# Optimization experiments

Measured on AMD Instinct MI355X. Metric: run time of the kernel, lower is better.

Reference implementation:

```python
import jax, jax.numpy as jnp
import numpy as np
import math

NEG = -1e9


def maximum_path(neg_cent, text_len, spec_len):
    # neg_cent: [B, Ts, Tt]; monotonic alignment (Viterbi) DP as in VITS.
    B, Ts, Tt = neg_cent.shape
    jj = jnp.arange(Tt)
    tt = jnp.arange(Ts)
    node_mask = (jj[None, None, :] < text_len[:, None, None]) & (tt[None, :, None] < spec_len[:, None, None])
    nc = jnp.where(node_mask, neg_cent, NEG)

    def fstep(q, nc_t):
        # q: [B, Tt] best score ending at text index j at previous frame
        q_shift = jnp.concatenate([jnp.full((B, 1), NEG, q.dtype), q[:, :-1]], axis=1)
        d = q_shift >= q  # True -> came from j-1 (diagonal move)
        q_new = nc_t + jnp.maximum(q, q_shift)
        return q_new, d

    q0 = jnp.broadcast_to(jnp.where(jj == 0, 0.0, NEG), (B, Tt)).astype(neg_cent.dtype)
    _, dirs = jax.lax.scan(fstep, q0, jnp.swapaxes(nc, 0, 1))  # dirs: [Ts, B, Tt]

    def bstep(j, inp):
        t, d_t = inp
        start = (t == spec_len - 1)
        j_eff = jnp.where(start, text_len - 1, j)
        valid = t < spec_len
        emit = ((jj[None, :] == j_eff[:, None]) & valid[:, None]).astype(neg_cent.dtype)
        came_diag = jnp.take_along_axis(d_t, j_eff[:, None], axis=1)[:, 0]
        j_next = jnp.where(valid, jnp.maximum(j_eff - came_diag.astype(j_eff.dtype), 0), j_eff)
        return j_next, emit

    j_init = jnp.zeros((B,), text_len.dtype)
    _, path = jax.lax.scan(bstep, j_init, (jnp.arange(Ts), dirs), reverse=True)
    return jnp.swapaxes(path, 0, 1)  # [B, Ts, Tt]


def setup_inputs() -> dict:
    B, C, Ts, Tt = 16, 192, 2048, 512
    key = jax.random.key(0)
    k1, k2, k3, k4, k5 = jax.random.split(key, 5)
    z_p = jax.random.normal(k1, (B, C, Ts), dtype=jnp.float32)
    m_p = jax.random.normal(k2, (B, C, Tt), dtype=jnp.float32)
    logs_p = 0.1 * jax.random.normal(k3, (B, C, Tt), dtype=jnp.float32)
    text_len = jax.random.randint(k4, (B,), Tt // 2, Tt + 1, dtype=jnp.int32)
    extra = jax.random.randint(k5, (B,), 0, Ts - Tt + 1, dtype=jnp.int32)
    spec_len = jnp.minimum(text_len + extra, Ts)
    return {"z_p": z_p, "m_p": m_p, "logs_p": logs_p, "spec_len": spec_len, "text_len": text_len}


def reference(z_p, m_p, logs_p, spec_len, text_len):
    B, C, Ts = z_p.shape
    Tt = m_p.shape[2]
    text_mask = (jnp.arange(Tt)[None, :] < text_len[:, None]).astype(z_p.dtype)[:, None, :]  # [B,1,Tt]
    spec_mask = (jnp.arange(Ts)[None, :] < spec_len[:, None]).astype(z_p.dtype)[:, None, :]  # [B,1,Ts]

    # --- neg_cent (torch.no_grad block) ---
    s_p_sq_r = jnp.exp(-2.0 * logs_p)  # [B,C,Tt]
    neg_cent1 = jnp.sum(-0.5 * math.log(2.0 * math.pi) - logs_p, axis=1, keepdims=True)  # [B,1,Tt]
    neg_cent2 = jnp.einsum('bct,bcu->btu', -0.5 * z_p ** 2, s_p_sq_r)  # [B,Ts,Tt]
    neg_cent3 = jnp.einsum('bct,bcu->btu', z_p, m_p * s_p_sq_r)  # [B,Ts,Tt]
    neg_cent4 = jnp.sum(-0.5 * m_p ** 2 * s_p_sq_r, axis=1, keepdims=True)  # [B,1,Tt]
    neg_cent = neg_cent1 + neg_cent2 + neg_cent3 + neg_cent4

    path = jax.lax.stop_gradient(maximum_path(neg_cent, text_len, spec_len))  # [B,Ts,Tt]

    duration = jnp.sum(path, axis=1)[:, None, :]  # [B,1,Tt]
    logw_ = jnp.log(duration + 1e-6) * text_mask  # [B,1,Tt]

    # expand prior stats along the alignment path: [B,C,Ts]
    m_p_exp = jnp.einsum('btu,bcu->bct', path, m_p)
    logs_p_exp = jnp.einsum('btu,bcu->bct', path, logs_p)

    return (path, duration, logw_, m_p_exp, logs_p_exp, text_mask, spec_mask)
```

## Files before the change

### kernel.cpp

```cpp
#include <hip/hip_runtime.h>
#include <hip/hip_bf16.h>
#include <math.h>

#define BB 16
#define CC 192
#define TS 2048
#define TT 512
#define KK 384

#define OFF_PATH 0
#define OFF_DUR  (16777216)
#define OFF_LOGW (OFF_DUR + 8192)
#define OFF_MEXP (OFF_LOGW + 8192)
#define OFF_LEXP (OFF_MEXP + 6291456)
#define OFF_TMASK (OFF_LEXP + 6291456)
#define OFF_SMASK (OFF_TMASK + 8192)

#define NEGCF (-1e9f)

__global__ __launch_bounds__(512) void vits_prep(
    const float* __restrict__ m_p, const float* __restrict__ logs_p,
    const int* __restrict__ spec_len, const int* __restrict__ text_len,
    float* __restrict__ Bmat, float* __restrict__ avec,
    float* __restrict__ tmask, float* __restrict__ smask)
{
    const int uc = blockIdx.x;
    const int b  = blockIdx.y;
    const int tid = threadIdx.x;
    const int ul = tid & 31;
    const int cg = tid >> 5;
    const int u = uc*32 + ul;
    const float C0 = -0.91893853320467274178f;
    float a_acc = 0.f;
    for (int c = cg; c < CC; c += 16) {
        float lg = logs_p[((size_t)b*CC + c)*TT + u];
        float mm = m_p[((size_t)b*CC + c)*TT + u];
        float s  = expf(-2.f*lg);
        float ms = mm * s;
        Bmat[((size_t)b*KK + 2*c    )*TT + u] = ms;
        Bmat[((size_t)b*KK + 2*c + 1)*TT + u] = s;
        a_acc += C0 - lg - 0.5f*mm*ms;
    }
    __shared__ float red[16][33];
    red[cg][ul] = a_acc;
    __syncthreads();
    #pragma unroll
    for (int s = 8; s > 0; s >>= 1) {
        if (cg < s) red[cg][ul] += red[cg + s][ul];
        __syncthreads();
    }
    if (cg == 0) {
        avec[b*TT + u] = red[0][ul];
        tmask[b*TT + u] = (u < text_len[b]) ? 1.f : 0.f;
    }
    if (tid < 128) {
        int t = uc*128 + tid;
        smask[b*TS + t] = (t < spec_len[b]) ? 1.f : 0.f;
    }
}

__global__ __launch_bounds__(256) void vits_gemm(
    const float* __restrict__ z, const float* __restrict__ Bmat,
    const float* __restrict__ avec, float* __restrict__ out)
{
    const int b  = blockIdx.z;
    const int t0 = blockIdx.y * 128;
    const int u0 = blockIdx.x * 128;
    __shared__ float As[8][128];
    __shared__ float Bs[8][128];
    const int tid = threadIdx.x;
    const int tx = tid & 15, ty = tid >> 4;
    float acc[8][8] = {};
    const float* zb = z    + (size_t)b * CC * TS;
    const float* Bb = Bmat + (size_t)b * KK * TT;

    const int c_l = tid >> 6;
    const int t_l = (tid & 63) * 2;
    const int k_b = tid >> 5;
    const int u_l = (tid & 31) * 4;

    float2 zr = *(const float2*)(zb + (size_t)c_l*TS + t0 + t_l);
    float4 br = *(const float4*)(Bb + (size_t)k_b*TT + u0 + u_l);

    for (int kc = 0; kc < KK/8; ++kc) {
        *(float2*)&As[2*c_l  ][t_l] = make_float2(zr.x, zr.y);
        *(float2*)&As[2*c_l+1][t_l] = make_float2(-0.5f*zr.x*zr.x, -0.5f*zr.y*zr.y);
        *(float4*)&Bs[k_b][u_l] = br;
        __syncthreads();
        if (kc + 1 < KK/8) {
            zr = *(const float2*)(zb + (size_t)((kc+1)*4 + c_l)*TS + t0 + t_l);
            br = *(const float4*)(Bb + (size_t)((kc+1)*8 + k_b)*TT + u0 + u_l);
        }
        #pragma unroll
        for (int k = 0; k < 8; ++k) {
            float4 a0 = *(const float4*)&As[k][ty*4];
            float4 a1 = *(const float4*)&As[k][ty*4 + 64];
            float4 b0 = *(const float4*)&Bs[k][tx*4];
            float4 b1 = *(const float4*)&Bs[k][tx*4 + 64];
            float aa[8] = {a0.x,a0.y,a0.z,a0.w,a1.x,a1.y,a1.z,a1.w};
            float bb[8] = {b0.x,b0.y,b0.z,b0.w,b1.x,b1.y,b1.z,b1.w};
            #pragma unroll
            for (int i = 0; i < 8; ++i)
                #pragma unroll
                for (int j = 0; j < 8; ++j)
                    acc[i][j] += aa[i]*bb[j];
        }
        __syncthreads();
    }

    float4 ab0 = *(const float4*)(avec + b*TT + u0 + tx*4);
    float4 ab1 = *(const float4*)(avec + b*TT + u0 + tx*4 + 64);
    float ab[8] = {ab0.x,ab0.y,ab0.z,ab0.w,ab1.x,ab1.y,ab1.z,ab1.w};
    #pragma unroll
    for (int i = 0; i < 8; ++i) {
        int tt = t0 + ((i < 4) ? (ty*4 + i) : (64 + ty*4 + (i-4)));
        float* orow = out + (size_t)((size_t)b*TS + tt)*TT + u0;
        float4 o0, o1;
        o0.x = acc[i][0] + ab[0]; o0.y = acc[i][1] + ab[1];
        o0.z = acc[i][2] + ab[2]; o0.w = acc[i][3] + ab[3];
        o1.x = acc[i][4] + ab[4]; o1.y = acc[i][5] + ab[5];
        o1.z = acc[i][6] + ab[6]; o1.w = acc[i][7] + ab[7];
        *(float4*)(orow + tx*4)      = o0;
        *(float4*)(orow + tx*4 + 64) = o1;
    }
}

__device__ __forceinline__ float dpp_ror1_f32(float v) {
    union { float f; int i; } u, r;
    u.f = v;
    r.i = __builtin_amdgcn_update_dpp(0, u.i, 0x13C, 0xF, 0xF, false);
    return r.f;
}

#define DIRS(j,w) dirs[((j)<<6) | ((w) ^ ((j) & 31))]
#define RING 16

__global__ __launch_bounds__(1024, 1) void vits_dp(
    const float* __restrict__ nc,
    const int* __restrict__ spec_len, const int* __restrict__ text_len,
    float* __restrict__ dur, float* __restrict__ logw, int* __restrict__ jt)
{
    __shared__ unsigned int dirs[TT*(TS/32)];
    __shared__ float qrow[TT];
    __shared__ int Tr[TT + 1];

    const int tid  = threadIdx.x;
    const int lane = tid & 63;
    const int wid  = tid >> 6;
    const int b = blockIdx.x;
    const int SL = spec_len[b], TL = text_len[b];
    const int col = (wid << 5) + lane - 32;
    const bool auth = (lane >= 32);
    const bool w0g  = (wid == 0) && (lane < 32);
    const int colL = (col < 0) ? 0 : col;

    float q = (col == 0) ? 0.0f : NEGCF;
    unsigned int bits = 0;

    const float* ncb = nc + (size_t)b*TS*TT + colL;

    float pf[RING];
    #pragma unroll
    for (int i = 0; i < RING; ++i) pf[i] = ncb[(size_t)i*TT];
    const float* pcur = ncb + (size_t)RING*TT;

    int tb = 0;
    for (; tb + 32 <= SL; tb += 32) {
        #pragma unroll
        for (int s = 0; s < 32; ++s) {
            const int t = tb + s;
            float f = pf[s & (RING-1)];
            pf[s & (RING-1)] = *pcur;
            pcur += TT;

            float qp = dpp_ror1_f32(q);
            bool d = (qp >= q);
            bits = (bits << 1) | (unsigned)d;
            float qn = f + fmaxf(qp, q);
            q = w0g ? NEGCF : qn;

            if (s == 31) {
                if (auth) {
                    DIRS(col, t >> 5) = bits;
                    qrow[col] = q;
                }
                bits = 0;
                __syncthreads();
                if (!auth && wid != 0) q = qrow[col];
                __syncthreads();
            }
        }
    }
    for (int t = tb; t < SL; ++t) {
        float f = ncb[(size_t)t*TT];
        float qp = dpp_ror1_f32(q);
        bool d = (qp >= q);
        bits = (bits << 1) | (unsigned)d;
        float qn = f + fmaxf(qp, q);
        q = w0g ? NEGCF : qn;
    }
    if (SL & 31) {
        int w = SL >> 5, r = SL & 31;
        if (auth) DIRS(col, w) = bits << (32 - r);
    }
    __syncthreads();

    for (int i = tid; i <= TT; i += 1024) Tr[i] = 0;
    __syncthreads();

    if (tid == 0) {
        Tr[TL] = SL;
        int j = TL - 1, tc = SL - 1;
        while (j > 0 && tc >= 0) {
            int w = tc >> 5;
            int bcur = 31 - (tc & 31);
            unsigned int W = DIRS(j, w) & (0xFFFFFFFFu << bcur);
            if (W) {
                int bp = __ffs(W) - 1;
                int tp = (w << 5) + 31 - bp;
                Tr[j] = tp;
                --j;
                tc = tp - 1;
            } else {
                if (w == 0) break;
                tc = (w << 5) - 1;
            }
        }
    }
    __syncthreads();

    for (int u = tid; u < TT; u += 1024) {
        float dv = (u < TL) ? (float)(Tr[u+1] - Tr[u]) : 0.0f;
        dur[b*TT + u] = dv;
        logw[b*TT + u] = (u < TL) ? logf(dv + 1e-6f) : 0.0f;
    }
    for (int u = 0; u < TL; ++u) {
        int t1 = Tr[u+1];
        for (int t = Tr[u] + tid; t < t1; t += 1024) jt[b*TS + t] = u;
    }
    for (int t = SL + tid; t < TS; t += 1024) jt[b*TS + t] = -1;
}

__global__ void vits_path(const int* __restrict__ jt, float4* __restrict__ path)
{
    int idx = blockIdx.x*blockDim.x + threadIdx.x;
    const int total = BB*TS*(TT/4);
    for (; idx < total; idx += gridDim.x*blockDim.x) {
        int u4 = idx & (TT/4 - 1);
        int bt = idx >> 7;
        int j = jt[bt];
        float4 v = make_float4(0.f,0.f,0.f,0.f);
        int r = j - (u4 << 2);
        if (r >= 0 && r < 4) ((float*)&v)[r] = 1.f;
        path[idx] = v;
    }
}

__global__ void vits_mlexp(const int* __restrict__ jt,
    const float* __restrict__ m_p, const float* __restrict__ logs_p,
    float4* __restrict__ mexp, float4* __restrict__ lexp)
{
    int idx = blockIdx.x*blockDim.x + threadIdx.x;
    const int total = BB*CC*(TS/4);
    for (; idx < total; idx += gridDim.x*blockDim.x) {
        int t4 = idx & (TS/4 - 1);
        int bc = idx >> 9;
        int b = bc / CC;
        int4 jv = *(const int4*)(jt + b*TS + (t4 << 2));
        const float* mrow = m_p    + (size_t)bc*TT;
        const float* lrow = logs_p + (size_t)bc*TT;
        float4 mv, lv;
        mv.x = (jv.x >= 0) ? mrow[jv.x] : 0.f;  lv.x = (jv.x >= 0) ? lrow[jv.x] : 0.f;
        mv.y = (jv.y >= 0) ? mrow[jv.y] : 0.f;  lv.y = (jv.y >= 0) ? lrow[jv.y] : 0.f;
        mv.z = (jv.z >= 0) ? mrow[jv.z] : 0.f;  lv.z = (jv.z >= 0) ? lrow[jv.z] : 0.f;
        mv.w = (jv.w >= 0) ? mrow[jv.w] : 0.f;  lv.w = (jv.w >= 0) ? lrow[jv.w] : 0.f;
        mexp[idx] = mv;
        lexp[idx] = lv;
    }
}

extern "C" void kernel_launch(void* const* d_in, const int* in_sizes, int n_in,
                              void* d_out, int out_size, void* d_ws, size_t ws_size,
                              hipStream_t stream) {
    const float* z_p      = (const float*)d_in[0];
    const float* m_p      = (const float*)d_in[1];
    const float* logs_p   = (const float*)d_in[2];
    const int*   spec_len = (const int*)d_in[3];
    const int*   text_len = (const int*)d_in[4];
    float* out = (float*)d_out;

    float* Bmat = (float*)d_ws;
    float* avec = Bmat + (size_t)BB*KK*TT;
    int*   jt   = (int*)(avec + BB*TT);

    float* path  = out + OFF_PATH;
    float* dur   = out + OFF_DUR;
    float* logw  = out + OFF_LOGW;
    float* mexp  = out + OFF_MEXP;
    float* lexp  = out + OFF_LEXP;
    float* tmask = out + OFF_TMASK;
    float* smask = out + OFF_SMASK;

    vits_prep<<<dim3(16, BB), 512, 0, stream>>>(m_p, logs_p, spec_len, text_len,
                                                Bmat, avec, tmask, smask);
    vits_gemm<<<dim3(TT/128, TS/128, BB), 256, 0, stream>>>(z_p, Bmat, avec, path);
    vits_dp<<<BB, 1024, 0, stream>>>(path, spec_len, text_len, dur, logw, jt);
    vits_path<<<2048, 256, 0, stream>>>(jt, (float4*)path);
    vits_mlexp<<<2048, 256, 0, stream>>>(jt, m_p, logs_p, (float4*)mexp, (float4*)lexp);
}
```

Baseline: 440.8 us.

## Store cost matrix in time-grouped layout and stream DP rows through LDS ring

The GEMM epilogue now writes neg_cent in a transposed layout that groups four consecutive time steps per text column, as float4. The DP kernel streams these groups into a three-slot LDS ring using global_load_lds with explicit waitcnt and barrier control, replacing the per-thread register prefetch ring. This gives the serial scan one LDS float4 read per four steps and overlaps global loads with compute. The cost is more barriers per window, strided float4 stores in the GEMM epilogue, and Tr reusing ring memory.

```diff
diff --git a/kernel.cpp b/kernel.cpp
--- a/kernel.cpp
+++ b/kernel.cpp
@@ -17,6 +17,7 @@
 #define OFF_SMASK (OFF_TMASK + 8192)
 
 #define NEGCF (-1e9f)
+#define GSTR (TT*4)
 
 __global__ __launch_bounds__(512) void vits_prep(
     const float* __restrict__ m_p, const float* __restrict__ logs_p,
@@ -61,7 +62,7 @@
 
 __global__ __launch_bounds__(256) void vits_gemm(
     const float* __restrict__ z, const float* __restrict__ Bmat,
-    const float* __restrict__ avec, float* __restrict__ out)
+    const float* __restrict__ avec, float* __restrict__ ncT)
 {
     const int b  = blockIdx.z;
     const int t0 = blockIdx.y * 128;
@@ -111,17 +112,19 @@
     float4 ab0 = *(const float4*)(avec + b*TT + u0 + tx*4);
     float4 ab1 = *(const float4*)(avec + b*TT + u0 + tx*4 + 64);
     float ab[8] = {ab0.x,ab0.y,ab0.z,ab0.w,ab1.x,ab1.y,ab1.z,ab1.w};
+    float* ncTb = ncT + (size_t)b*(TS/4)*GSTR;
+    const int g1 = (t0 >> 2) + ty;
+    const int g2 = g1 + 16;
     #pragma unroll
-    for (int i = 0; i < 8; ++i) {
-        int tt = t0 + ((i < 4) ? (ty*4 + i) : (64 + ty*4 + (i-4)));
-        float* orow = out + (size_t)((size_t)b*TS + tt)*TT + u0;
-        float4 o0, o1;
-        o0.x = acc[i][0] + ab[0]; o0.y = acc[i][1] + ab[1];
-        o0.z = acc[i][2] + ab[2]; o0.w = acc[i][3] + ab[3];
-        o1.x = acc[i][4] + ab[4]; o1.y = acc[i][5] + ab[5];
-        o1.z = acc[i][6] + ab[6]; o1.w = acc[i][7] + ab[7];
-        *(float4*)(orow + tx*4)      = o0;
-        *(float4*)(orow + tx*4 + 64) = o1;
+    for (int jj = 0; jj < 8; ++jj) {
+        int u = u0 + ((jj < 4) ? (tx*4 + jj) : (64 + tx*4 + (jj-4)));
+        float4 lo, hi;
+        lo.x = acc[0][jj]+ab[jj]; lo.y = acc[1][jj]+ab[jj];
+        lo.z = acc[2][jj]+ab[jj]; lo.w = acc[3][jj]+ab[jj];
+        hi.x = acc[4][jj]+ab[jj]; hi.y = acc[5][jj]+ab[jj];
+        hi.z = acc[6][jj]+ab[jj]; hi.w = acc[7][jj]+ab[jj];
+        *(float4*)(ncTb + ((size_t)g1*TT + u)*4) = lo;
+        *(float4*)(ncTb + ((size_t)g2*TT + u)*4) = hi;
     }
 }
 
@@ -132,17 +135,20 @@
     return r.f;
 }
 
+#define GLDS(srcp, dstp) __builtin_amdgcn_global_load_lds( \
+    (const __attribute__((address_space(1))) unsigned int*)(srcp), \
+    (__attribute__((address_space(3))) unsigned int*)(dstp), 4, 0, 0)
+
 #define DIRS(j,w) dirs[((j)<<6) | ((w) ^ ((j) & 31))]
-#define RING 16
 
 __global__ __launch_bounds__(1024, 1) void vits_dp(
-    const float* __restrict__ nc,
+    const float* __restrict__ ncT,
     const int* __restrict__ spec_len, const int* __restrict__ text_len,
     float* __restrict__ dur, float* __restrict__ logw, int* __restrict__ jt)
 {
     __shared__ unsigned int dirs[TT*(TS/32)];
+    __shared__ float ring[3][2048];
     __shared__ float qrow[TT];
-    __shared__ int Tr[TT + 1];
 
     const int tid  = threadIdx.x;
     const int lane = tid & 63;
@@ -157,42 +163,58 @@
     float q = (col == 0) ? 0.0f : NEGCF;
     unsigned int bits = 0;
 
-    const float* ncb = nc + (size_t)b*TS*TT + colL;
-
-    float pf[RING];
-    #pragma unroll
-    for (int i = 0; i < RING; ++i) pf[i] = ncb[(size_t)i*TT];
-    const float* pcur = ncb + (size_t)RING*TT;
-
-    int tb = 0;
-    for (; tb + 32 <= SL; tb += 32) {
+    const char* ncB = (const char*)ncT + (size_t)b*(TS/4)*8192;
+    const int stoff = wid*512 + (lane << 2);
+
+    const int nwin = SL >> 2;
+
+    {
+        const char* s0 = ncB + stoff;
+        GLDS(s0,        (char*)&ring[0][0] + stoff);
+        GLDS(s0 + 256,  (char*)&ring[0][0] + stoff + 256);
+        const char* s1 = ncB + 8192 + stoff;
+        GLDS(s1,        (char*)&ring[1][0] + stoff);
+        GLDS(s1 + 256,  (char*)&ring[1][0] + stoff + 256);
+    }
+    asm volatile("s_waitcnt vmcnt(0)" ::: "memory");
+    __syncthreads();
+
+    int slot = 0;
+    for (int k = 0; k < nwin; ++k) {
+        asm volatile("s_barrier" ::: "memory");
+        {
+            int g = k + 2; if (g > TS/4 - 1) g = TS/4 - 1;
+            int s2 = slot + 2; if (s2 >= 3) s2 -= 3;
+            const char* sp = ncB + (size_t)g*8192 + stoff;
+            char* dp_ = (char*)&ring[0][0] + s2*8192 + stoff;
+            GLDS(sp,       dp_);
+            GLDS(sp + 256, dp_ + 256);
+        }
+        const float4 f4 = *(const float4*)((const char*)&ring[0][0] + slot*8192 + (colL << 4));
         #pragma unroll
-        for (int s = 0; s < 32; ++s) {
-            const int t = tb + s;
-            float f = pf[s & (RING-1)];
-            pf[s & (RING-1)] = *pcur;
-            pcur += TT;
-
+        for (int s = 0; s < 4; ++s) {
+            float f = ((const float*)&f4)[s];
             float qp = dpp_ror1_f32(q);
             bool d = (qp >= q);
             bits = (bits << 1) | (unsigned)d;
             float qn = f + fmaxf(qp, q);
             q = w0g ? NEGCF : qn;
-
-            if (s == 31) {
-                if (auth) {
-                    DIRS(col, t >> 5) = bits;
-                    qrow[col] = q;
-                }
-                bits = 0;
-                __syncthreads();
-                if (!auth && wid != 0) q = qrow[col];
-                __syncthreads();
+        }
+        if ((k & 7) == 7) {
+            if (auth) {
+                DIRS(col, (4*k+3) >> 5) = bits;
+                qrow[col] = q;
             }
-        }
-    }
-    for (int t = tb; t < SL; ++t) {
-        float f = ncb[(size_t)t*TT];
+            bits = 0;
+            asm volatile("s_waitcnt lgkmcnt(0)" ::: "memory");
+            asm volatile("s_barrier" ::: "memory");
+            if (!auth && wid) q = qrow[col];
+        }
+        asm volatile("s_waitcnt vmcnt(2)" ::: "memory");
+        slot = (slot + 1 == 3) ? 0 : slot + 1;
+    }
+    for (int t = nwin*4; t < SL; ++t) {
+        float f = *(const float*)(ncB + ((size_t)(t >> 2)*8192) + (colL << 4) + ((t & 3) << 2));
         float qp = dpp_ror1_f32(q);
         bool d = (qp >= q);
         bits = (bits << 1) | (unsigned)d;
@@ -205,6 +227,7 @@
     }
     __syncthreads();
 
+    int* Tr = (int*)&ring[0][0];
     for (int i = tid; i <= TT; i += 1024) Tr[i] = 0;
     __syncthreads();
 
```

New measurement: 618.0 us. 40.2% more time.

## Replace block barriers in DP with wavefront-pipelined LDS boundary handoff

Applied to the files above, without the earlier changes.

The Viterbi forward pass previously used 16 waves with 32-column overlap and two block-wide barriers every 32 frames. It now uses 8 waves that each own 64 distinct columns. Each wave passes its boundary column to the next wave through an LDS ring buffer and signals progress with per-wave flags, so waves run as a skewed software pipeline without block barriers. This removes the redundant overlap work and the barrier stalls. In exchange it relies on spin-waits with volatile LDS flags and a bounded ring, which adds ordering risk and a pipeline fill delay across waves.

```diff
diff --git a/kernel.cpp b/kernel.cpp
--- a/kernel.cpp
+++ b/kernel.cpp
@@ -133,15 +133,15 @@
 }
 
 #define DIRS(j,w) dirs[((j)<<6) | ((w) ^ ((j) & 31))]
-#define RING 16
-
-__global__ __launch_bounds__(1024, 1) void vits_dp(
+
+__global__ __launch_bounds__(512, 1) void vits_dp(
     const float* __restrict__ nc,
     const int* __restrict__ spec_len, const int* __restrict__ text_len,
     float* __restrict__ dur, float* __restrict__ logw, int* __restrict__ jt)
 {
     __shared__ unsigned int dirs[TT*(TS/32)];
-    __shared__ float qrow[TT];
+    __shared__ float bq[8][256];
+    __shared__ int prog[8];
     __shared__ int Tr[TT + 1];
 
     const int tid  = threadIdx.x;
@@ -149,63 +149,83 @@
     const int wid  = tid >> 6;
     const int b = blockIdx.x;
     const int SL = spec_len[b], TL = text_len[b];
-    const int col = (wid << 5) + lane - 32;
-    const bool auth = (lane >= 32);
-    const bool w0g  = (wid == 0) && (lane < 32);
-    const int colL = (col < 0) ? 0 : col;
+    const int col = (wid << 6) + lane;
+    const bool l0  = (lane == 0);
+    const bool l63 = (lane == 63);
 
     float q = (col == 0) ? 0.0f : NEGCF;
     unsigned int bits = 0;
 
-    const float* ncb = nc + (size_t)b*TS*TT + colL;
-
-    float pf[RING];
+    const float* ncb = nc + (size_t)b*TS*TT + col;
+    float pf[16];
     #pragma unroll
-    for (int i = 0; i < RING; ++i) pf[i] = ncb[(size_t)i*TT];
-    const float* pcur = ncb + (size_t)RING*TT;
-
-    int tb = 0;
-    for (; tb + 32 <= SL; tb += 32) {
+    for (int i = 0; i < 16; ++i) pf[i] = ncb[(size_t)i*TT];
+    const float* pcur = ncb + (size_t)16*TT;
+
+    for (int i = tid; i < 8*256; i += 512) ((float*)bq)[i] = NEGCF;
+    if (tid < 8) prog[tid] = 0;
+    __syncthreads();
+
+    volatile int* vprog = (volatile int*)prog;
+    const int nch = SL >> 5;
+
+    for (int c = 0; c < nch; ++c) {
+        if (wid > 0) { while (vprog[wid-1] < c+1) __builtin_amdgcn_s_sleep(1); }
+        if (wid < 7 && c > 6) { while (vprog[wid+1] < c-6) __builtin_amdgcn_s_sleep(1); }
+        asm volatile("" ::: "memory");
+
+        float4 R[9];
+        R[0] = *(const float4*)&bq[wid][(c*32 + 252) & 255];
+        #pragma unroll
+        for (int g = 1; g < 9; ++g)
+            R[g] = *(const float4*)&bq[wid][(c*32 + (g-1)*4) & 255];
+
+        float4 wbuf;
         #pragma unroll
         for (int s = 0; s < 32; ++s) {
-            const int t = tb + s;
-            float f = pf[s & (RING-1)];
-            pf[s & (RING-1)] = *pcur;
+            float f = pf[s & 15];
+            pf[s & 15] = *pcur;
             pcur += TT;
-
-            float qp = dpp_ror1_f32(q);
-            bool d = (qp >= q);
+            float B = ((const float*)&R[(s+3) >> 2])[(s+3) & 3];
+            float qr = dpp_ror1_f32(q);
+            float qprev = l0 ? B : qr;
+            bool d = (qprev >= q);
             bits = (bits << 1) | (unsigned)d;
-            float qn = f + fmaxf(qp, q);
-            q = w0g ? NEGCF : qn;
-
-            if (s == 31) {
-                if (auth) {
-                    DIRS(col, t >> 5) = bits;
-                    qrow[col] = q;
-                }
-                bits = 0;
-                __syncthreads();
-                if (!auth && wid != 0) q = qrow[col];
-                __syncthreads();
+            q = f + fmaxf(qprev, q);
+            ((float*)&wbuf)[s & 3] = q;
+            if ((s & 3) == 3) {
+                if (l63 && wid < 7)
+                    *(float4*)&bq[wid+1][(c*32 + s - 3) & 255] = wbuf;
             }
         }
-    }
-    for (int t = tb; t < SL; ++t) {
-        float f = ncb[(size_t)t*TT];
-        float qp = dpp_ror1_f32(q);
-        bool d = (qp >= q);
-        bits = (bits << 1) | (unsigned)d;
-        float qn = f + fmaxf(qp, q);
-        q = w0g ? NEGCF : qn;
-    }
-    if (SL & 31) {
-        int w = SL >> 5, r = SL & 31;
-        if (auth) DIRS(col, w) = bits << (32 - r);
-    }
-    __syncthreads();
-
-    for (int i = tid; i <= TT; i += 1024) Tr[i] = 0;
+        DIRS(col, c) = bits;
+        bits = 0;
+        asm volatile("s_waitcnt lgkmcnt(0)" ::: "memory");
+        if (l0) vprog[wid] = c + 1;
+    }
+
+    const int rem = SL & 31;
+    if (rem) {
+        if (wid > 0) { while (vprog[wid-1] < nch+1) __builtin_amdgcn_s_sleep(1); }
+        asm volatile("" ::: "memory");
+        for (int t = nch*32; t < SL; ++t) {
+            float f = ncb[(size_t)t*TT];
+            float B = *(volatile float*)&bq[wid][(t-1) & 255];
+            float qr = dpp_ror1_f32(q);
+            float qprev = l0 ? B : qr;
+            bool d = (qprev >= q);
+            bits = (bits << 1) | (unsigned)d;
+            q = f + fmaxf(qprev, q);
+            if (l63 && wid < 7) *(volatile float*)&bq[wid+1][t & 255] = q;
+            asm volatile("s_waitcnt lgkmcnt(0)" ::: "memory");
+        }
+        DIRS(col, SL >> 5) = bits << (32 - rem);
+        asm volatile("s_waitcnt lgkmcnt(0)" ::: "memory");
+        if (l0) vprog[wid] = nch + 1;
+    }
+    __syncthreads();
+
+    for (int i = tid; i <= TT; i += 512) Tr[i] = 0;
     __syncthreads();
 
     if (tid == 0) {
@@ -229,16 +249,16 @@
     }
     __syncthreads();
 
-    for (int u = tid; u < TT; u += 1024) {
+    for (int u = tid; u < TT; u += 512) {
         float dv = (u < TL) ? (float)(Tr[u+1] - Tr[u]) : 0.0f;
         dur[b*TT + u] = dv;
         logw[b*TT + u] = (u < TL) ? logf(dv + 1e-6f) : 0.0f;
     }
     for (int u = 0; u < TL; ++u) {
         int t1 = Tr[u+1];
-        for (int t = Tr[u] + tid; t < t1; t += 1024) jt[b*TS + t] = u;
-    }
-    for (int t = SL + tid; t < TS; t += 1024) jt[b*TS + t] = -1;
+        for (int t = Tr[u] + tid; t < t1; t += 512) jt[b*TS + t] = u;
+    }
+    for (int t = SL + tid; t < TS; t += 512) jt[b*TS + t] = -1;
 }
 
 __global__ void vits_path(const int* __restrict__ jt, float4* __restrict__ path)
@@ -304,7 +324,7 @@
     vits_prep<<<dim3(16, BB), 512, 0, stream>>>(m_p, logs_p, spec_len, text_len,
                                                 Bmat, avec, tmask, smask);
     vits_gemm<<<dim3(TT/128, TS/128, BB), 256, 0, stream>>>(z_p, Bmat, avec, path);
-    vits_dp<<<BB, 1024, 0, stream>>>(path, spec_len, text_len, dur, logw, jt);
+    vits_dp<<<BB, 512, 0, stream>>>(path, spec_len, text_len, dur, logw, jt);
     vits_path<<<2048, 256, 0, stream>>>(jt, (float4*)path);
     vits_mlexp<<<2048, 256, 0, stream>>>(jt, m_p, logs_p, (float4*)mexp, (float4*)lexp);
 }
```

Result: faster. 426.4 us (-3.3%).
